# Optimization experiments

Hardware: AMD Instinct MI355X
Metric: run time of the kernel (lower is better)

Reference implementation:

```python
import jax, jax.numpy as jnp
import numpy as np
import math

B, H, W = 4, 256, 256
S = 256          # num_superpixels
ZD = 128         # z_dim
GC = 256         # g_channels
NBLK = 8


def setup_inputs() -> dict:
    key = jax.random.key(0)
    ks = jax.random.split(key, 12)
    rn = lambda k, shp, s=1.0: jax.random.normal(k, shp, jnp.float32) * s
    return {
        "z": rn(ks[0], (B, ZD)),
        "images": rn(ks[1], (B, 3, H, W)),
        "segments": jax.random.randint(ks[2], (B, H, W), 0, S).astype(jnp.int32),
        # row-stochastic-ish adjacency scale keeps 8 propagations stable
        "A": rn(ks[3], (B, S, S), 1.0 / math.sqrt(S)),
        # WSConv2d weights: init N(0,1); forward multiplies input by sqrt(2/(in*k*k))
        "proj_w": rn(ks[4], (GC, 3 + ZD)), "proj_b": jnp.zeros((GC,), jnp.float32),
        "blk_proj_w": rn(ks[5], (NBLK, GC, GC)), "blk_proj_b": jnp.zeros((NBLK, GC), jnp.float32),
        "ada1_w": rn(ks[6], (NBLK, 2 * GC, GC)), "ada1_b": jnp.zeros((NBLK, 2 * GC), jnp.float32),
        "ada2_w": rn(ks[7], (NBLK, 2 * GC, 2 * GC)), "ada2_b": jnp.zeros((NBLK, 2 * GC), jnp.float32),
        # plain Conv2d 3x3 layers in upsample head
        "up1_w": rn(ks[8], (GC // 2, GC, 3, 3), 0.02), "up1_b": jnp.zeros((GC // 2,), jnp.float32),
        "up2_w": rn(ks[9], (3, GC // 2, 3, 3), 0.02), "up2_b": jnp.zeros((3,), jnp.float32),
    }


def _ws1x1(x, w, b):
    # WSConv2d with 1x1 kernel over node dim: x [B,Cin,S] -> [B,Cout,S]
    scale = math.sqrt(2.0 / w.shape[1])
    return jnp.einsum('oc,bcs->bos', w, x) * scale + b[None, :, None]


def _conv3(x, w, b):
    y = jax.lax.conv_general_dilated(x, w, (1, 1), 'SAME',
                                     dimension_numbers=('NCHW', 'OIHW', 'NCHW'))
    return y + b[None, :, None, None]


def _forward(z, images, A, proj_w, proj_b, blk_proj_w, blk_proj_b,
             ada1_w, ada1_b, ada2_w, ada2_b, up1_w, up1_b, up2_w, up2_b,
             segments):
    Bn, _, Hn, Wn = images.shape
    N = Hn * Wn
    flat = images.reshape(Bn, 3, N)            # [B,3,N]
    seg = segments.reshape(Bn, N)              # [B,N] int

    # superpixel mean pooling (math of one_hot^T @ flat / counts, as segment-sum)
    seg_sum = jax.vmap(lambda f, s: jax.ops.segment_sum(f, s, num_segments=S))(
        flat.transpose(0, 2, 1), seg)          # [B,S,3]
    counts = jax.vmap(lambda s: jax.ops.segment_sum(
        jnp.ones(s.shape, jnp.float32), s, num_segments=S))(seg)  # [B,S]
    feats = seg_sum / (counts[..., None] + 1e-6)

    z_rep = jnp.broadcast_to(z[:, None, :], (Bn, S, ZD))
    x = jnp.concatenate([feats, z_rep], axis=2).transpose(0, 2, 1)  # [B,3+ZD,S]
    x = _ws1x1(x, proj_w, proj_b)                                   # [B,GC,S]

    for i in range(NBLK):
        h = _ws1x1(x, blk_proj_w[i], blk_proj_b[i])
        # A @ feat : out[b,c,i] = sum_j A[b,i,j] h[b,c,j]
        h = jnp.einsum('bij,bcj->bci', A, h)
        # AdaIN: style from global mean over nodes
        m = h.mean(axis=2, keepdims=True)                    # [B,GC,1]
        s1 = jax.nn.leaky_relu(_ws1x1(m, ada1_w[i], ada1_b[i]), 0.2)
        style = _ws1x1(s1, ada2_w[i], ada2_b[i])             # [B,2GC,1]
        gamma, beta = jnp.split(style, 2, axis=1)
        h = gamma * h + beta
        x = jax.nn.leaky_relu(h, 0.2)                        # dropout=0 (eval)

    # broadcast superpixel feats back to pixels (math of one_hot @ sup_feats)
    sup_feats = x.transpose(0, 2, 1)                         # [B,S,GC]
    pix = jnp.take_along_axis(sup_feats, seg[:, :, None].astype(jnp.int32), axis=1)  # [B,N,GC]
    pix = pix.transpose(0, 2, 1).reshape(Bn, GC, Hn, Wn)

    y = jax.nn.leaky_relu(_conv3(pix, up1_w, up1_b), 0.2)
    y = _conv3(y, up2_w, up2_b)                              # [B,3,H,W]
    # InstanceNorm2d(3), affine=False, eps=1e-5
    mu = y.mean((2, 3), keepdims=True)
    var = y.var((2, 3), keepdims=True)
    y = (y - mu) / jnp.sqrt(var + 1e-5)
    return jnp.tanh(y)


def reference(z, images, segments, A, proj_w, proj_b, blk_proj_w, blk_proj_b,
              ada1_w, ada1_b, ada2_w, ada2_b, up1_w, up1_b, up2_w, up2_b):
    return _forward(z, images, A, proj_w, proj_b, blk_proj_w, blk_proj_b,
                    ada1_w, ada1_b, ada2_w, ada2_b, up1_w, up1_b, up2_w, up2_b,
                    segments)
```

## Files before the change

kernel.cpp:

```cpp
#include <hip/hip_runtime.h>
#include <cmath>

#define BB 4
#define SS 256
#define ZDIM 128
#define GCH 256
#define NBLKS 8
#define NPIX 65536
#define U1C 128

__device__ __forceinline__ float lrelu(float x){ return x >= 0.f ? x : 0.2f*x; }

__global__ void k_pool(const float* __restrict__ img, const int* __restrict__ seg,
                       float* __restrict__ segsum, float* __restrict__ counts){
  __shared__ float ls[SS*4];
  int t = threadIdx.x;
  for(int j=t;j<SS*4;j+=256) ls[j]=0.f;
  __syncthreads();
  int b = blockIdx.x >> 6;
  int base = blockIdx.x*1024;
  for(int it=0; it<4; it++){
    int idx = base + it*256 + t;
    int n = idx & (NPIX-1);
    int s = seg[idx];
    atomicAdd(&ls[s*4+0], img[(b*3+0)*NPIX+n]);
    atomicAdd(&ls[s*4+1], img[(b*3+1)*NPIX+n]);
    atomicAdd(&ls[s*4+2], img[(b*3+2)*NPIX+n]);
    atomicAdd(&ls[s*4+3], 1.0f);
  }
  __syncthreads();
  for(int j=t;j<SS*4;j+=256){
    int s = j>>2, c = j&3;
    float vv = ls[j];
    if(vv != 0.f){
      if(c<3) atomicAdd(&segsum[(b*SS+s)*3+c], vv);
      else    atomicAdd(&counts[b*SS+s], vv);
    }
  }
}

__global__ __launch_bounds__(256) void k_prepA(const float* __restrict__ A,
                                               float* __restrict__ At){
  __shared__ float t[32][33];
  int b = blockIdx.z;
  int bx = blockIdx.x*32, by = blockIdx.y*32;
  int lx = threadIdx.x & 31, ly4 = (threadIdx.x >> 5)*4;
  #pragma unroll
  for(int r=0;r<4;r++)
    t[ly4+r][lx] = A[(b<<16) + ((by+ly4+r)<<8) + bx + lx];
  __syncthreads();
  #pragma unroll
  for(int r=0;r<4;r++)
    At[(b<<16) + ((bx+ly4+r)<<8) + by + lx] = t[lx][ly4+r];
}

__global__ void k_prepW(const float* __restrict__ w1, const float* __restrict__ w2,
                        float* __restrict__ wT, float* __restrict__ w2t){
  int idx = blockIdx.x*256 + threadIdx.x;
  if(idx < 294912){
    int o = idx & 127; int r = idx >> 7; int c = r & 255; int k = r >> 8;
    wT[idx] = w1[(o*GCH + c)*9 + k];
  } else if(idx < 294912 + 3456){
    int t = idx - 294912;
    int cc = t & 7;
    int oc = (t >> 3) % 3;
    int sg = (t / 24) & 3;
    int g  = (t / 96) & 3;
    int k  = t / 384;
    w2t[t] = w2[oc*1152 + (g*32 + sg*8 + cc)*9 + k];
  }
}

__global__ void k_x0(const float* __restrict__ segsum, const float* __restrict__ counts,
                     const float* __restrict__ z, const float* __restrict__ pw,
                     const float* __restrict__ pb, float sc, float* __restrict__ xp){
  int i = blockIdx.x*64 + (threadIdx.x & 63);
  int o = blockIdx.y*4  + (threadIdx.x >> 6);
  int b = blockIdx.z;
  float cnt = counts[b*SS+i] + 1e-6f;
  float f0 = segsum[(b*SS+i)*3+0]/cnt;
  float f1 = segsum[(b*SS+i)*3+1]/cnt;
  float f2 = segsum[(b*SS+i)*3+2]/cnt;
  const float* wr = pw + o*131;
  float acc = wr[0]*f0 + wr[1]*f1 + wr[2]*f2;
  const float* zb = z + b*ZDIM;
  #pragma unroll 8
  for(int j=0;j<ZDIM;j++) acc += wr[3+j]*zb[j];
  xp[(b*GCH+o)*SS + i] = acc*sc + pb[o];
}

__global__ __launch_bounds__(512) void k_gemm(const float* __restrict__ xp,
        const float* __restrict__ bw, const float* __restrict__ bb,
        const float* __restrict__ At, float sc,
        float* __restrict__ h2, float* __restrict__ m){
  int c0 = blockIdx.x*4;
  int b  = blockIdx.y;
  int j  = threadIdx.x & 255;
  int half = threadIdx.x >> 8;
  __shared__ float wl[4][256];
  __shared__ float h1l[4][260];
  __shared__ float red[4][4];
  wl[half*2+0][j] = bw[(c0+half*2+0)*GCH + j];
  wl[half*2+1][j] = bw[(c0+half*2+1)*GCH + j];
  __syncthreads();
  const float* xb = xp + b*GCH*SS + j;
  float a0 = 0.f, a1 = 0.f;
  int ch = half*2;
  #pragma unroll 8
  for(int k=0;k<GCH;k++){
    float xv = xb[k*SS];
    a0 += wl[ch][k]*xv;
    a1 += wl[ch+1][k]*xv;
  }
  h1l[ch][j]   = a0*sc + bb[c0+ch];
  h1l[ch+1][j] = a1*sc + bb[c0+ch+1];
  __syncthreads();
  const float* ab = At + b*SS*SS + j;
  float r0 = 0.f, r1 = 0.f;
  #pragma unroll 2
  for(int jj=0;jj<SS;jj+=4){
    float4 h0 = *(const float4*)&h1l[ch][jj];
    float4 h1v = *(const float4*)&h1l[ch+1][jj];
    float av0 = ab[jj*SS], av1 = ab[(jj+1)*SS], av2 = ab[(jj+2)*SS], av3 = ab[(jj+3)*SS];
    r0 += h0.x*av0 + h0.y*av1 + h0.z*av2 + h0.w*av3;
    r1 += h1v.x*av0 + h1v.y*av1 + h1v.z*av2 + h1v.w*av3;
  }
  h2[(b*GCH+c0+ch)*SS + j]   = r0;
  h2[(b*GCH+c0+ch+1)*SS + j] = r1;
  float s0 = r0, s1v = r1;
  for(int off=32; off; off>>=1){ s0 += __shfl_down(s0,off); s1v += __shfl_down(s1v,off); }
  int w3 = (threadIdx.x >> 6) & 3;
  if((j&63)==0){ red[ch][w3] = s0; red[ch+1][w3] = s1v; }
  __syncthreads();
  if(threadIdx.x < 4)
    m[b*GCH + c0 + threadIdx.x] =
      (red[threadIdx.x][0]+red[threadIdx.x][1]+red[threadIdx.x][2]+red[threadIdx.x][3])*(1.f/256.f);
}

__global__ __launch_bounds__(512) void k_s12(const float* __restrict__ m,
        const float* __restrict__ a1w, const float* __restrict__ a1b,
        const float* __restrict__ a2w, const float* __restrict__ a2b,
        const float* __restrict__ h2, float sc1, float sc2, float* __restrict__ xp){
  int q = blockIdx.x;
  int tid = threadIdx.x;
  int lane = tid & 63, wv = tid >> 6;
  int grp = lane >> 3, ll = lane & 7;
  __shared__ float4 ml4[256];
  __shared__ float s1l[4][512];
  __shared__ float gbl[4][16];
  if(tid < 256) ml4[tid] = ((const float4*)m)[tid];
  __syncthreads();
  #pragma unroll 2
  for(int pass=0; pass<8; pass++){
    int row = wv*64 + pass*8 + grp;
    const float4* ar = (const float4*)(a1w + row*GCH) + ll;
    float p0=0.f,p1=0.f,p2=0.f,p3=0.f;
    #pragma unroll
    for(int j=0;j<8;j++){
      float4 w4 = ar[j*8];
      float4 m0 = ml4[0*64 + j*8 + ll];
      float4 m1 = ml4[1*64 + j*8 + ll];
      float4 m2 = ml4[2*64 + j*8 + ll];
      float4 m3 = ml4[3*64 + j*8 + ll];
      p0 += w4.x*m0.x + w4.y*m0.y + w4.z*m0.z + w4.w*m0.w;
      p1 += w4.x*m1.x + w4.y*m1.y + w4.z*m1.z + w4.w*m1.w;
      p2 += w4.x*m2.x + w4.y*m2.y + w4.z*m2.z + w4.w*m2.w;
      p3 += w4.x*m3.x + w4.y*m3.y + w4.z*m3.z + w4.w*m3.w;
    }
    #pragma unroll
    for(int off=1; off<8; off<<=1){
      p0 += __shfl_xor(p0,off); p1 += __shfl_xor(p1,off);
      p2 += __shfl_xor(p2,off); p3 += __shfl_xor(p3,off);
    }
    if(ll == 0){
      float bv = a1b[row];
      int sidx = ((row & 7) << 6) + (row >> 3);
      s1l[0][sidx] = lrelu(p0*sc1 + bv);
      s1l[1][sidx] = lrelu(p1*sc1 + bv);
      s1l[2][sidx] = lrelu(p2*sc1 + bv);
      s1l[3][sidx] = lrelu(p3*sc1 + bv);
    }
  }
  __syncthreads();
  float sA[4][8];
  #pragma unroll
  for(int b=0;b<4;b++)
    #pragma unroll
    for(int j=0;j<8;j++) sA[b][j] = s1l[b][j*64 + lane];
  #pragma unroll
  for(int r=0;r<2;r++){
    int ridx = wv*2 + r;
    int cc = ridx & 7;
    int t = (ridx < 8) ? (q*8 + cc) : (256 + q*8 + cc);
    const float* wr = a2w + t*512 + lane*8;
    float4 wa = *(const float4*)wr;
    float4 wb4 = *(const float4*)(wr+4);
    float p0 = wa.x*sA[0][0]+wa.y*sA[0][1]+wa.z*sA[0][2]+wa.w*sA[0][3]
             + wb4.x*sA[0][4]+wb4.y*sA[0][5]+wb4.z*sA[0][6]+wb4.w*sA[0][7];
    float p1 = wa.x*sA[1][0]+wa.y*sA[1][1]+wa.z*sA[1][2]+wa.w*sA[1][3]
             + wb4.x*sA[1][4]+wb4.y*sA[1][5]+wb4.z*sA[1][6]+wb4.w*sA[1][7];
    float p2 = wa.x*sA[2][0]+wa.y*sA[2][1]+wa.z*sA[2][2]+wa.w*sA[2][3]
             + wb4.x*sA[2][4]+wb4.y*sA[2][5]+wb4.z*sA[2][6]+wb4.w*sA[2][7];
    float p3 = wa.x*sA[3][0]+wa.y*sA[3][1]+wa.z*sA[3][2]+wa.w*sA[3][3]
             + wb4.x*sA[3][4]+wb4.y*sA[3][5]+wb4.z*sA[3][6]+wb4.w*sA[3][7];
    for(int off=32; off; off>>=1){
      p0 += __shfl_xor(p0,off); p1 += __shfl_xor(p1,off);
      p2 += __shfl_xor(p2,off); p3 += __shfl_xor(p3,off);
    }
    if(lane < 4){
      float p = lane==0 ? p0 : lane==1 ? p1 : lane==2 ? p2 : p3;
      gbl[lane][ridx] = p*sc2 + a2b[t];
    }
  }
  __syncthreads();
  int c0 = q*8;
  int jn = tid & 255;
  int hf = tid >> 8;
  #pragma unroll
  for(int b=0;b<4;b++){
    #pragma unroll
    for(int c2=0;c2<4;c2++){
      int cc = hf*4 + c2;
      float ga = gbl[b][cc], be = gbl[b][8+cc];
      float hv = h2[(b*GCH + c0+cc)*SS + jn];
      xp[(b*GCH + c0+cc)*SS + jn] = lrelu(ga*hv + be);
    }
  }
}

__global__ __launch_bounds__(256) void k_v(const float* __restrict__ xf,
        const float4* __restrict__ wT4, float4* __restrict__ v4){
  int s0 = blockIdx.x*16;
  int k  = blockIdx.y;
  int b  = blockIdx.z;
  int tid = threadIdx.x;
  __shared__ float4 wl[64][33];
  __shared__ float xft[256][16];
  for(int t = tid; t < 1024; t += 256){
    int c = t>>2, sf = t&3;
    *(float4*)&xft[c][sf*4] = *(const float4*)(xf + (b*GCH+c)*SS + s0 + sf*4);
  }
  int og = tid & 31, sh = tid >> 5;
  const float4* wb = wT4 + (size_t)k*GCH*32;
  float4 a0 = {0.f,0.f,0.f,0.f}, a1 = {0.f,0.f,0.f,0.f};
  for(int ct=0; ct<4; ct++){
    __syncthreads();
    for(int t = tid; t < 2048; t += 256){
      int cc = t>>5, o = t&31;
      wl[cc][o] = wb[(ct*64+cc)*32 + o];
    }
    __syncthreads();
    #pragma unroll 4
    for(int cc=0;cc<64;cc++){
      float4 w = wl[cc][og];
      int c = ct*64+cc;
      float x0v = xft[c][sh];
      float x1v = xft[c][8+sh];
      a0.x += w.x*x0v; a0.y += w.y*x0v; a0.z += w.z*x0v; a0.w += w.w*x0v;
      a1.x += w.x*x1v; a1.y += w.y*x1v; a1.z += w.z*x1v; a1.w += w.w*x1v;
    }
  }
  size_t base = (size_t)(b*9+k)*SS + s0;
  v4[(base + sh)*32 + og]     = a0;
  v4[(base + 8 + sh)*32 + og] = a1;
}

__global__ __launch_bounds__(256) void k_conv(const float4* __restrict__ v4,
        const int* __restrict__ seg, const float4* __restrict__ b14,
        const float* __restrict__ w2t, float* __restrict__ y2){
  __shared__ float4 y1t4[100*9];
  __shared__ int   segl[144];
  __shared__ float part[768];
  int bid = blockIdx.x;
  int x = bid & 7;
  int b = x >> 1;
  int sub = ((bid >> 3) << 1) + (x & 1);
  int g = sub & 3;
  int tile = sub >> 2;
  int x0p = (tile & 31)*8, y0p = (tile >> 5)*8;
  int tid = threadIdx.x;
  if(tid < 144){
    int r = tid/12, cc = tid%12;
    int gy = y0p - 2 + r, gx = x0p - 2 + cc;
    segl[tid] = (gy>=0 && gy<256 && gx>=0 && gx<256) ? seg[(b*256+gy)*256+gx] : -1;
  }
  __syncthreads();
  int o4 = tid & 7;
  const float4* vb = v4 + (size_t)(b*9)*SS*32 + g*8 + o4;
  float4 bias = b14[g*8 + o4];
  bool interior = (x0p >= 8 && x0p <= 240 && y0p >= 8 && y0p <= 240);
  if(interior){
    for(int task = tid; task < 800; task += 256){
      int pp = task >> 3;
      int py = pp/10, px = pp - py*10;
      float4 acc = bias;
      #pragma unroll
      for(int k=0;k<9;k++){
        int sidx = segl[(py + k/3)*12 + (px + k%3)];
        float4 vv = vb[(k*SS + sidx)*32];
        acc.x += vv.x; acc.y += vv.y; acc.z += vv.z; acc.w += vv.w;
      }
      float4 val;
      val.x = lrelu(acc.x); val.y = lrelu(acc.y);
      val.z = lrelu(acc.z); val.w = lrelu(acc.w);
      y1t4[pp*9 + o4] = val;
    }
  } else {
    for(int task = tid; task < 800; task += 256){
      int pp = task >> 3;
      int py = pp/10, px = pp - py*10;
      int gy = y0p - 1 + py, gx = x0p - 1 + px;
      bool pix_ok = (gy>=0 && gy<256 && gx>=0 && gx<256);
      float4 acc = bias;
      #pragma unroll
      for(int k=0;k<9;k++){
        int sidx = segl[(py + k/3)*12 + (px + k%3)];
        int sidx0 = sidx < 0 ? 0 : sidx;
        float msk = sidx < 0 ? 0.f : 1.f;
        float4 vv = vb[(k*SS + sidx0)*32];
        acc.x += msk*vv.x; acc.y += msk*vv.y; acc.z += msk*vv.z; acc.w += msk*vv.w;
      }
      float4 val;
      val.x = pix_ok ? lrelu(acc.x) : 0.f;
      val.y = pix_ok ? lrelu(acc.y) : 0.f;
      val.z = pix_ok ? lrelu(acc.z) : 0.f;
      val.w = pix_ok ? lrelu(acc.w) : 0.f;
      y1t4[pp*9 + o4] = val;
    }
  }
  __syncthreads();
  int pxo = tid & 63, sg = tid >> 6;
  int sgu = __builtin_amdgcn_readfirstlane(sg);
  const float* wk0 = w2t + (g*4 + sgu)*24;
  int ty = pxo >> 3, tx = pxo & 7;
  float p0=0.f,p1=0.f,p2=0.f;
  #pragma unroll
  for(int k=0;k<9;k++){
    int pp0 = (ty + k/3)*10 + (tx + k%3);
    float4 ya = y1t4[pp0*9 + sgu*2];
    float4 yb = y1t4[pp0*9 + sgu*2 + 1];
    const float* wk = wk0 + k*384;
    p0 += wk[0]*ya.x + wk[1]*ya.y + wk[2]*ya.z + wk[3]*ya.w
        + wk[4]*yb.x + wk[5]*yb.y + wk[6]*yb.z + wk[7]*yb.w;
    p1 += wk[8]*ya.x + wk[9]*ya.y + wk[10]*ya.z + wk[11]*ya.w
        + wk[12]*yb.x + wk[13]*yb.y + wk[14]*yb.z + wk[15]*yb.w;
    p2 += wk[16]*ya.x + wk[17]*ya.y + wk[18]*ya.z + wk[19]*ya.w
        + wk[20]*yb.x + wk[21]*yb.y + wk[22]*yb.z + wk[23]*yb.w;
  }
  part[tid]     = p0;
  part[256+tid] = p1;
  part[512+tid] = p2;
  __syncthreads();
  if(tid < 64){
    float s0 = part[tid]    +part[tid+64]    +part[tid+128]    +part[tid+192];
    float s1 = part[256+tid]+part[256+tid+64]+part[256+tid+128]+part[256+tid+192];
    float s2 = part[512+tid]+part[512+tid+64]+part[512+tid+128]+part[512+tid+192];
    int gy = y0p + (tid>>3), gx = x0p + (tid&7);
    int nidx = gy*256+gx;
    atomicAdd(&y2[(b*3+0)*NPIX+nidx], s0);
    atomicAdd(&y2[(b*3+1)*NPIX+nidx], s1);
    atomicAdd(&y2[(b*3+2)*NPIX+nidx], s2);
  }
}

__global__ void k_stats(const float* __restrict__ y2, double* __restrict__ stats){
  int bc = blockIdx.x;
  int chunk = blockIdx.y;
  const float* p = y2 + (size_t)bc*NPIX + chunk*8192;
  int t = threadIdx.x;
  double s=0.0, q=0.0;
  for(int i=t;i<8192;i+=256){ double vv = (double)p[i]; s+=vv; q+=vv*vv; }
  __shared__ double rs[256], rq[256];
  rs[t]=s; rq[t]=q; __syncthreads();
  for(int st=128; st; st>>=1){ if(t<st){rs[t]+=rs[t+st]; rq[t]+=rq[t+st];} __syncthreads(); }
  if(t==0){ atomicAdd(&stats[bc*2], rs[0]); atomicAdd(&stats[bc*2+1], rq[0]); }
}

__global__ void k_norm(const float* __restrict__ y2, const double* __restrict__ stats,
                       float* __restrict__ out){
  int idx = blockIdx.x*256+threadIdx.x;
  int bu = idx >> 16;
  double mu  = stats[bu*2+0] * (1.0/65536.0);
  double ex2 = stats[bu*2+1] * (1.0/65536.0);
  double var = ex2 - mu*mu;
  float inv = (float)(1.0/sqrt(var + 1e-5));
  float mf = (float)mu;
  out[idx] = tanhf((y2[idx]-mf)*inv);
}

extern "C" void kernel_launch(void* const* d_in, const int* in_sizes, int n_in,
                              void* d_out, int out_size, void* d_ws, size_t ws_size,
                              hipStream_t stream) {
  const float* z   = (const float*)d_in[0];
  const float* img = (const float*)d_in[1];
  const int*   seg = (const int*)d_in[2];
  const float* A   = (const float*)d_in[3];
  const float* pw  = (const float*)d_in[4];
  const float* pb  = (const float*)d_in[5];
  const float* bw  = (const float*)d_in[6];
  const float* bb  = (const float*)d_in[7];
  const float* a1w = (const float*)d_in[8];
  const float* a1b = (const float*)d_in[9];
  const float* a2w = (const float*)d_in[10];
  const float* a2b = (const float*)d_in[11];
  const float* w1  = (const float*)d_in[12];
  const float* b1  = (const float*)d_in[13];
  const float* w2  = (const float*)d_in[14];
  const float* b2  = (const float*)d_in[15]; (void)b2;
  float* out = (float*)d_out;

  float* ws = (float*)d_ws;
  float* segsum = ws;
  float* counts = ws + 3072;
  float* m      = ws + 4096;
  double* stats = (double*)(ws + 5120);
  float* xp  = ws + 5248;
  float* h2  = xp + 262144;
  float* At  = h2 + 262144;
  float* wT  = At + 262144;
  float* v   = wT + 294912;
  float* y2  = v + 1179648;
  float* w2t = y2 + 786432;

  hipMemsetAsync(ws, 0, 5248*sizeof(float), stream);
  hipMemsetAsync(y2, 0, 786432*sizeof(float), stream);

  float sProj = (float)sqrt(2.0/131.0);
  float s256  = (float)sqrt(2.0/256.0);
  float s512  = (float)sqrt(2.0/512.0);

  k_pool <<<256, 256, 0, stream>>>(img, seg, segsum, counts);
  k_prepA<<<dim3(8,8,4), 256, 0, stream>>>(A, At);
  k_prepW<<<1166, 256, 0, stream>>>(w1, w2, wT, w2t);
  k_x0   <<<dim3(4,64,4), 256, 0, stream>>>(segsum, counts, z, pw, pb, sProj, xp);

  for(int blk=0; blk<NBLKS; blk++){
    k_gemm<<<dim3(64,4), 512, 0, stream>>>(xp, bw + blk*GCH*GCH, bb + blk*GCH,
                                           At, s256, h2, m);
    k_s12 <<<32, 512, 0, stream>>>(m, a1w + blk*512*GCH, a1b + blk*512,
                                   a2w + blk*512*512, a2b + blk*512,
                                   h2, s256, s512, xp);
  }

  k_v   <<<dim3(16,9,4), 256, 0, stream>>>(xp, (const float4*)wT, (float4*)v);
  k_conv<<<16384, 256, 0, stream>>>((const float4*)v, seg, (const float4*)b1, w2t, y2);
  k_stats<<<dim3(12,8), 256, 0, stream>>>(y2, stats);
  k_norm<<<3072, 256, 0, stream>>>(y2, stats, out);
}
```

Measured before the change: 408.7 us.

## Batch conv gathers, transpose LDS layout, reorder tile mapping, merge prep kernels

Several changes at once. The k_conv first-stage gather now keeps four independent accumulators per thread so the nine-tap gather loads for all of a thread's pixels can be in flight together. The y1 LDS tile moves to a channel-major layout padded to 101 to change bank access in the second conv stage. The block-to-tile mapping now puts the channel group in the high bits, so consecutive blocks share a group and its slice of v in cache. k_prepA and k_prepW are merged into one launch, and k_norm computes its batch index per block; the cost is higher register pressure in k_conv.

```diff
diff --git a/kernel.cpp b/kernel.cpp
--- a/kernel.cpp
+++ b/kernel.cpp
@@ -39,35 +39,36 @@
   }
 }
 
-__global__ __launch_bounds__(256) void k_prepA(const float* __restrict__ A,
-                                               float* __restrict__ At){
-  __shared__ float t[32][33];
-  int b = blockIdx.z;
-  int bx = blockIdx.x*32, by = blockIdx.y*32;
-  int lx = threadIdx.x & 31, ly4 = (threadIdx.x >> 5)*4;
-  #pragma unroll
-  for(int r=0;r<4;r++)
-    t[ly4+r][lx] = A[(b<<16) + ((by+ly4+r)<<8) + bx + lx];
-  __syncthreads();
-  #pragma unroll
-  for(int r=0;r<4;r++)
-    At[(b<<16) + ((bx+ly4+r)<<8) + by + lx] = t[lx][ly4+r];
-}
-
-__global__ void k_prepW(const float* __restrict__ w1, const float* __restrict__ w2,
-                        float* __restrict__ wT, float* __restrict__ w2t){
-  int idx = blockIdx.x*256 + threadIdx.x;
-  if(idx < 294912){
-    int o = idx & 127; int r = idx >> 7; int c = r & 255; int k = r >> 8;
-    wT[idx] = w1[(o*GCH + c)*9 + k];
-  } else if(idx < 294912 + 3456){
-    int t = idx - 294912;
-    int cc = t & 7;
-    int oc = (t >> 3) % 3;
-    int sg = (t / 24) & 3;
-    int g  = (t / 96) & 3;
-    int k  = t / 384;
-    w2t[t] = w2[oc*1152 + (g*32 + sg*8 + cc)*9 + k];
+__global__ __launch_bounds__(256) void k_prep(const float* __restrict__ A,
+        const float* __restrict__ w1, const float* __restrict__ w2,
+        float* __restrict__ At, float* __restrict__ wT, float* __restrict__ w2t){
+  int bid = blockIdx.x;
+  if(bid < 256){
+    __shared__ float t[32][33];
+    int b = bid >> 6;
+    int bx = (bid & 7)*32, by = ((bid >> 3) & 7)*32;
+    int lx = threadIdx.x & 31, ly4 = (threadIdx.x >> 5)*4;
+    #pragma unroll
+    for(int r=0;r<4;r++)
+      t[ly4+r][lx] = A[(b<<16) + ((by+ly4+r)<<8) + bx + lx];
+    __syncthreads();
+    #pragma unroll
+    for(int r=0;r<4;r++)
+      At[(b<<16) + ((bx+ly4+r)<<8) + by + lx] = t[lx][ly4+r];
+  } else {
+    int idx = (bid-256)*256 + threadIdx.x;
+    if(idx < 294912){
+      int o = idx & 127; int r = idx >> 7; int c = r & 255; int k = r >> 8;
+      wT[idx] = w1[(o*GCH + c)*9 + k];
+    } else if(idx < 294912 + 3456){
+      int t2 = idx - 294912;
+      int cc = t2 & 7;
+      int oc = (t2 >> 3) % 3;
+      int sg = (t2 / 24) & 3;
+      int g  = (t2 / 96) & 3;
+      int k  = t2 / 384;
+      w2t[t2] = w2[oc*1152 + (g*32 + sg*8 + cc)*9 + k];
+    }
   }
 }
 
@@ -268,15 +269,15 @@
 __global__ __launch_bounds__(256) void k_conv(const float4* __restrict__ v4,
         const int* __restrict__ seg, const float4* __restrict__ b14,
         const float* __restrict__ w2t, float* __restrict__ y2){
-  __shared__ float4 y1t4[100*9];
+  __shared__ float4 y1t4[8*101];
   __shared__ int   segl[144];
   __shared__ float part[768];
   int bid = blockIdx.x;
   int x = bid & 7;
   int b = x >> 1;
   int sub = ((bid >> 3) << 1) + (x & 1);
-  int g = sub & 3;
-  int tile = sub >> 2;
+  int g = sub >> 10;
+  int tile = sub & 1023;
   int x0p = (tile & 31)*8, y0p = (tile >> 5)*8;
   int tid = threadIdx.x;
   if(tid < 144){
@@ -288,44 +289,73 @@
   int o4 = tid & 7;
   const float4* vb = v4 + (size_t)(b*9)*SS*32 + g*8 + o4;
   float4 bias = b14[g*8 + o4];
+  int ppv[4], sbase[4];
+  bool tval[4];
+  #pragma unroll
+  for(int t=0;t<4;t++){
+    int task = tid + t*256;
+    tval[t] = task < 800;
+    int p = task >> 3;
+    ppv[t] = p;
+    int py = p/10, px = p - py*10;
+    sbase[t] = py*12 + px;
+  }
+  float4 acc[4];
+  #pragma unroll
+  for(int t=0;t<4;t++) acc[t] = bias;
   bool interior = (x0p >= 8 && x0p <= 240 && y0p >= 8 && y0p <= 240);
   if(interior){
-    for(int task = tid; task < 800; task += 256){
-      int pp = task >> 3;
-      int py = pp/10, px = pp - py*10;
-      float4 acc = bias;
+    #pragma unroll
+    for(int k=0;k<9;k++){
+      const float4* vk = vb + k*SS*32;
       #pragma unroll
-      for(int k=0;k<9;k++){
-        int sidx = segl[(py + k/3)*12 + (px + k%3)];
-        float4 vv = vb[(k*SS + sidx)*32];
-        acc.x += vv.x; acc.y += vv.y; acc.z += vv.z; acc.w += vv.w;
+      for(int t=0;t<4;t++){
+        if(tval[t]){
+          int sidx = segl[sbase[t] + (k/3)*12 + (k%3)];
+          float4 vv = vk[sidx*32];
+          acc[t].x += vv.x; acc[t].y += vv.y; acc[t].z += vv.z; acc[t].w += vv.w;
+        }
       }
-      float4 val;
-      val.x = lrelu(acc.x); val.y = lrelu(acc.y);
-      val.z = lrelu(acc.z); val.w = lrelu(acc.w);
-      y1t4[pp*9 + o4] = val;
+    }
+    #pragma unroll
+    for(int t=0;t<4;t++){
+      if(tval[t]){
+        float4 val;
+        val.x = lrelu(acc[t].x); val.y = lrelu(acc[t].y);
+        val.z = lrelu(acc[t].z); val.w = lrelu(acc[t].w);
+        y1t4[o4*101 + ppv[t]] = val;
+      }
     }
   } else {
-    for(int task = tid; task < 800; task += 256){
-      int pp = task >> 3;
-      int py = pp/10, px = pp - py*10;
-      int gy = y0p - 1 + py, gx = x0p - 1 + px;
-      bool pix_ok = (gy>=0 && gy<256 && gx>=0 && gx<256);
-      float4 acc = bias;
+    #pragma unroll
+    for(int k=0;k<9;k++){
+      const float4* vk = vb + k*SS*32;
       #pragma unroll
-      for(int k=0;k<9;k++){
-        int sidx = segl[(py + k/3)*12 + (px + k%3)];
-        int sidx0 = sidx < 0 ? 0 : sidx;
-        float msk = sidx < 0 ? 0.f : 1.f;
-        float4 vv = vb[(k*SS + sidx0)*32];
-        acc.x += msk*vv.x; acc.y += msk*vv.y; acc.z += msk*vv.z; acc.w += msk*vv.w;
+      for(int t=0;t<4;t++){
+        if(tval[t]){
+          int sidx = segl[sbase[t] + (k/3)*12 + (k%3)];
+          int sidx0 = sidx < 0 ? 0 : sidx;
+          float msk = sidx < 0 ? 0.f : 1.f;
+          float4 vv = vk[sidx0*32];
+          acc[t].x += msk*vv.x; acc[t].y += msk*vv.y;
+          acc[t].z += msk*vv.z; acc[t].w += msk*vv.w;
+        }
       }
-      float4 val;
-      val.x = pix_ok ? lrelu(acc.x) : 0.f;
-      val.y = pix_ok ? lrelu(acc.y) : 0.f;
-      val.z = pix_ok ? lrelu(acc.z) : 0.f;
-      val.w = pix_ok ? lrelu(acc.w) : 0.f;
-      y1t4[pp*9 + o4] = val;
+    }
+    #pragma unroll
+    for(int t=0;t<4;t++){
+      if(tval[t]){
+        int p = ppv[t];
+        int py = p/10, px = p - py*10;
+        int gy = y0p - 1 + py, gx = x0p - 1 + px;
+        bool pix_ok = (gy>=0 && gy<256 && gx>=0 && gx<256);
+        float4 val;
+        val.x = pix_ok ? lrelu(acc[t].x) : 0.f;
+        val.y = pix_ok ? lrelu(acc[t].y) : 0.f;
+        val.z = pix_ok ? lrelu(acc[t].z) : 0.f;
+        val.w = pix_ok ? lrelu(acc[t].w) : 0.f;
+        y1t4[o4*101 + p] = val;
+      }
     }
   }
   __syncthreads();
@@ -337,8 +367,8 @@
   #pragma unroll
   for(int k=0;k<9;k++){
     int pp0 = (ty + k/3)*10 + (tx + k%3);
-    float4 ya = y1t4[pp0*9 + sgu*2];
-    float4 yb = y1t4[pp0*9 + sgu*2 + 1];
+    float4 ya = y1t4[(sgu*2)*101 + pp0];
+    float4 yb = y1t4[(sgu*2+1)*101 + pp0];
     const float* wk = wk0 + k*384;
     p0 += wk[0]*ya.x + wk[1]*ya.y + wk[2]*ya.z + wk[3]*ya.w
         + wk[4]*yb.x + wk[5]*yb.y + wk[6]*yb.z + wk[7]*yb.w;
@@ -378,13 +408,13 @@
 
 __global__ void k_norm(const float* __restrict__ y2, const double* __restrict__ stats,
                        float* __restrict__ out){
-  int idx = blockIdx.x*256+threadIdx.x;
-  int bu = idx >> 16;
+  int bu = (blockIdx.x*256) >> 16;
   double mu  = stats[bu*2+0] * (1.0/65536.0);
   double ex2 = stats[bu*2+1] * (1.0/65536.0);
   double var = ex2 - mu*mu;
   float inv = (float)(1.0/sqrt(var + 1e-5));
   float mf = (float)mu;
+  int idx = blockIdx.x*256+threadIdx.x;
   out[idx] = tanhf((y2[idx]-mf)*inv);
 }
 
@@ -429,10 +459,9 @@
   float s256  = (float)sqrt(2.0/256.0);
   float s512  = (float)sqrt(2.0/512.0);
 
-  k_pool <<<256, 256, 0, stream>>>(img, seg, segsum, counts);
-  k_prepA<<<dim3(8,8,4), 256, 0, stream>>>(A, At);
-  k_prepW<<<1166, 256, 0, stream>>>(w1, w2, wT, w2t);
-  k_x0   <<<dim3(4,64,4), 256, 0, stream>>>(segsum, counts, z, pw, pb, sProj, xp);
+  k_pool<<<256, 256, 0, stream>>>(img, seg, segsum, counts);
+  k_prep<<<256 + 1166, 256, 0, stream>>>(A, w1, w2, At, wT, w2t);
+  k_x0  <<<dim3(4,64,4), 256, 0, stream>>>(segsum, counts, z, pw, pb, sProj, xp);
 
   for(int blk=0; blk<NBLKS; blk++){
     k_gemm<<<dim3(64,4), 512, 0, stream>>>(xp, bw + blk*GCH*GCH, bb + blk*GCH,
```

Result: slower. 426.4 us (+4.3%).
